# Kernel optimization log

Hardware: AMD Instinct MI355X
Metric: run time of the kernel (lower is better)

## Reference

```python
import jax, jax.numpy as jnp
import numpy as np

N, M, D = 4096, 8192, 512

def setup_inputs() -> dict:
    key = jax.random.key(0)
    k1, k2, k3, k4 = jax.random.split(key, 4)
    X = jax.random.normal(k1, (N, D), dtype=jnp.float32)
    SV = jax.random.normal(k2, (M, D), dtype=jnp.float32)
    DC = jax.random.normal(k3, (1, M), dtype=jnp.float32)
    IC = jax.random.normal(k4, (1,), dtype=jnp.float32)
    gamma = jnp.float32(1.0 / D)
    return {"X": X, "SV": SV, "DC": DC, "IC": IC, "gamma": gamma}

def reference(X, SV, DC, IC, gamma):
    # Squared pairwise L2 distances via GEMM expansion (same math as
    # ||SV - x||^2 without materializing the [N, M, D] broadcast tensor):
    # d2[n, m] = ||x_n||^2 + ||sv_m||^2 - 2 * x_n . sv_m
    x2 = jnp.sum(X * X, axis=1)          # [N]
    sv2 = jnp.sum(SV * SV, axis=1)       # [M]
    cross = jnp.einsum("nd,md->nm", X, SV)  # [N, M]
    d2 = jnp.maximum(x2[:, None] + sv2[None, :] - 2.0 * cross, 0.0)
    k = jnp.exp(-gamma * d2)             # RBF kernel values [N, M]
    # Weighted reduction over support vectors + intercept -> decision values [N]
    return jnp.sum(k * DC, axis=1) + IC
```

## Files before the change

### kernel.cpp

```cpp
#include <hip/hip_runtime.h>
#include <stdint.h>

#define NN 4096
#define MM 8192
#define DD 512
#define KT2 16

typedef __bf16 bf16x8 __attribute__((ext_vector_type(8)));
typedef __bf16 bf16x4 __attribute__((ext_vector_type(4)));
typedef float f32x4 __attribute__((ext_vector_type(4)));
typedef float f32x16 __attribute__((ext_vector_type(16)));

__device__ __forceinline__ void load_lds16(const void* g, void* l) {
  __builtin_amdgcn_global_load_lds(
      (const __attribute__((address_space(1))) unsigned int*)g,
      (__attribute__((address_space(3))) unsigned int*)l, 16, 0, 0);
}

__global__ __launch_bounds__(256) void convert_norm_kernel(
    const float* __restrict__ X, const float* __restrict__ SV,
    __bf16* __restrict__ Xb, __bf16* __restrict__ SVb,
    float* __restrict__ x2, float* __restrict__ sv2,
    float* __restrict__ out, const float* __restrict__ IC) {
  int wid = blockIdx.x * 4 + (threadIdx.x >> 6);
  int lane = threadIdx.x & 63;
  const float* src;
  __bf16* dst;
  float* nrm;
  if (wid < NN) {
    src = X + (size_t)wid * DD;
    dst = Xb + (size_t)wid * DD;
    nrm = x2 + wid;
    if (lane == 0) out[wid] = IC[0];
  } else {
    int r = wid - NN;
    src = SV + (size_t)r * DD;
    dst = SVb + (size_t)r * DD;
    nrm = sv2 + r;
  }
  const f32x4* s = (const f32x4*)src;
  f32x4 a = s[lane];
  f32x4 b = s[lane + 64];
  float sum = a.x * a.x + a.y * a.y + a.z * a.z + a.w * a.w +
              b.x * b.x + b.y * b.y + b.z * b.z + b.w * b.w;
  bf16x4 ca = {(__bf16)a.x, (__bf16)a.y, (__bf16)a.z, (__bf16)a.w};
  bf16x4 cb = {(__bf16)b.x, (__bf16)b.y, (__bf16)b.z, (__bf16)b.w};
  *(bf16x4*)(dst + 4 * lane) = ca;
  *(bf16x4*)(dst + 256 + 4 * lane) = cb;
#pragma unroll
  for (int m = 32; m >= 1; m >>= 1) sum += __shfl_xor(sum, m, 64);
  if (lane == 0) *nrm = sum;
}

__global__ __launch_bounds__(256, 4) void rbf_gemm_kernel(
    const bf16x8* __restrict__ Xb, const bf16x8* __restrict__ SVb,
    const float* __restrict__ x2, const float* __restrict__ sv2,
    const float* __restrict__ DC, const float* __restrict__ gamma_p,
    float* __restrict__ out) {
  __shared__ bf16x8 As[2][512];
  __shared__ bf16x8 Bs[2][512];

  const int t = threadIdx.x;
  const int lane = t & 63;
  const int wave = t >> 6;
  const int n0 = blockIdx.x * 128;
  const int m0 = blockIdx.y * 128;

  const int wave_m = wave & 1;
  const int wave_n = wave >> 1;
  const int l31 = lane & 31;
  const int lhi = lane >> 5;

  const int c0 = t;
  const int c1 = t + 256;
  const int r0 = c0 >> 2, k0 = (c0 & 3) ^ (r0 & 3);
  const int r1 = c1 >> 2, k1 = (c1 & 3) ^ (r1 & 3);
  const size_t gA0 = (size_t)(n0 + r0) * 64 + k0;
  const size_t gA1 = (size_t)(n0 + r1) * 64 + k1;
  const size_t gB0 = (size_t)(m0 + r0) * 64 + k0;
  const size_t gB1 = (size_t)(m0 + r1) * 64 + k1;

  const int ra4 = (wave_n * 64 + l31) * 4;
  const int rb4 = (wave_m * 64 + l31) * 4;

  f32x16 acc[2][2];
#pragma unroll
  for (int i = 0; i < 2; ++i)
#pragma unroll
    for (int j = 0; j < 2; ++j)
#pragma unroll
      for (int r = 0; r < 16; ++r) acc[i][j][r] = 0.0f;

  load_lds16(Xb + gA0, &As[0][c0]);
  load_lds16(Xb + gA1, &As[0][c1]);
  load_lds16(SVb + gB0, &Bs[0][c0]);
  load_lds16(SVb + gB1, &Bs[0][c1]);
  __syncthreads();

#pragma unroll
  for (int kt = 0; kt < KT2; ++kt) {
    const int cur = kt & 1;
    const int nxt = cur ^ 1;
    if (kt + 1 < KT2) {
      const int ko = (kt + 1) * 4;
      load_lds16(Xb + gA0 + ko, &As[nxt][c0]);
      load_lds16(Xb + gA1 + ko, &As[nxt][c1]);
      load_lds16(SVb + gB0 + ko, &Bs[nxt][c0]);
      load_lds16(SVb + gB1 + ko, &Bs[nxt][c1]);
    }
#pragma unroll
    for (int ks = 0; ks < 2; ++ks) {
      const int kc = ks * 2 + lhi;
      const int sw = kc ^ (l31 & 3);
      bf16x8 af0 = As[cur][ra4 + sw];
      bf16x8 af1 = As[cur][ra4 + 128 + sw];
      bf16x8 bf0 = Bs[cur][rb4 + sw];
      bf16x8 bf1 = Bs[cur][rb4 + 128 + sw];
      acc[0][0] = __builtin_amdgcn_mfma_f32_32x32x16_bf16(af0, bf0, acc[0][0], 0, 0, 0);
      acc[0][1] = __builtin_amdgcn_mfma_f32_32x32x16_bf16(af0, bf1, acc[0][1], 0, 0, 0);
      acc[1][0] = __builtin_amdgcn_mfma_f32_32x32x16_bf16(af1, bf0, acc[1][0], 0, 0, 0);
      acc[1][1] = __builtin_amdgcn_mfma_f32_32x32x16_bf16(af1, bf1, acc[1][1], 0, 0, 0);
    }
    __syncthreads();
  }

  const float g = gamma_p[0];
  const float c2 = g * 1.4426950408889634f;

  float sv2v[2], dcv[2];
  const int colb = m0 + wave_m * 64 + l31;
  sv2v[0] = sv2[colb];
  dcv[0] = DC[colb];
  sv2v[1] = sv2[colb + 32];
  dcv[1] = DC[colb + 32];

#pragma unroll
  for (int i = 0; i < 2; ++i) {
    const int rowb = n0 + wave_n * 64 + i * 32 + 4 * lhi;
    float val[16];
#pragma unroll
    for (int g4 = 0; g4 < 4; ++g4) {
      f32x4 xv = *(const f32x4*)(x2 + rowb + 8 * g4);
#pragma unroll
      for (int r2 = 0; r2 < 4; ++r2) {
        const int reg = g4 * 4 + r2;
        float v = 0.0f;
#pragma unroll
        for (int j = 0; j < 2; ++j) {
          float d2 = xv[r2] + sv2v[j] - 2.0f * acc[i][j][reg];
          d2 = fmaxf(d2, 0.0f);
          v += exp2f(-c2 * d2) * dcv[j];
        }
        val[reg] = v;
      }
    }
#pragma unroll
    for (int m = 1; m < 32; m <<= 1)
#pragma unroll
      for (int reg = 0; reg < 16; ++reg)
        val[reg] += __shfl_xor(val[reg], m, 64);
    if (l31 == 0) {
#pragma unroll
      for (int g4 = 0; g4 < 4; ++g4)
#pragma unroll
        for (int r2 = 0; r2 < 4; ++r2)
          atomicAdd(&out[rowb + 8 * g4 + r2], val[g4 * 4 + r2]);
    }
  }
}

extern "C" void kernel_launch(void* const* d_in, const int* in_sizes, int n_in,
                              void* d_out, int out_size, void* d_ws, size_t ws_size,
                              hipStream_t stream) {
  const float* X = (const float*)d_in[0];
  const float* SV = (const float*)d_in[1];
  const float* DC = (const float*)d_in[2];
  const float* IC = (const float*)d_in[3];
  const float* gamma = (const float*)d_in[4];
  float* out = (float*)d_out;

  char* ws = (char*)d_ws;
  __bf16* Xb = (__bf16*)ws;
  __bf16* SVb = (__bf16*)(ws + (size_t)NN * DD * 2);
  float* x2 = (float*)(ws + (size_t)(NN + MM) * DD * 2);
  float* sv2 = x2 + NN;

  convert_norm_kernel<<<(NN + MM) / 4, 256, 0, stream>>>(X, SV, Xb, SVb, x2, sv2, out, IC);
  dim3 grid(NN / 128, MM / 128);
  rbf_gemm_kernel<<<grid, 256, 0, stream>>>((const bf16x8*)Xb, (const bf16x8*)SVb,
                                            x2, sv2, DC, gamma, out);
}
```

Measured before the change: 144.5 us.

## Double block M-tile to 256 rows with 512 threads and pair-row LDS swizzle

Each workgroup of the fused bf16 MFMA GEMM now covers 256 rows of X instead of 128 and runs 8 waves instead of 4. Each SV tile loaded into LDS is therefore shared by twice as many rows, which cuts global B-tile traffic and halves the number of blocks. The LDS XOR swizzle now keys on row pairs, (row>>1)&3, rather than row&3, to change the bank-access pattern on fragment reads. In exchange, the 512-thread launch bound with 4 blocks per CU caps registers per thread, and the larger LDS footprint may lower occupancy.

Result: no change. 143.8 us (-0.5%).

```diff
diff --git a/kernel.cpp b/kernel.cpp
--- a/kernel.cpp
+++ b/kernel.cpp
@@ -4,7 +4,7 @@
 #define NN 4096
 #define MM 8192
 #define DD 512
-#define KT2 16
+#define KT3 16
 
 typedef __bf16 bf16x8 __attribute__((ext_vector_type(8)));
 typedef __bf16 bf16x4 __attribute__((ext_vector_type(4)));
@@ -52,18 +52,18 @@
   if (lane == 0) *nrm = sum;
 }
 
-__global__ __launch_bounds__(256, 4) void rbf_gemm_kernel(
+__global__ __launch_bounds__(512, 4) void rbf_gemm_kernel(
     const bf16x8* __restrict__ Xb, const bf16x8* __restrict__ SVb,
     const float* __restrict__ x2, const float* __restrict__ sv2,
     const float* __restrict__ DC, const float* __restrict__ gamma_p,
     float* __restrict__ out) {
-  __shared__ bf16x8 As[2][512];
+  __shared__ bf16x8 As[2][1024];
   __shared__ bf16x8 Bs[2][512];
 
   const int t = threadIdx.x;
   const int lane = t & 63;
   const int wave = t >> 6;
-  const int n0 = blockIdx.x * 128;
+  const int n0 = blockIdx.x * 256;
   const int m0 = blockIdx.y * 128;
 
   const int wave_m = wave & 1;
@@ -71,17 +71,17 @@
   const int l31 = lane & 31;
   const int lhi = lane >> 5;
 
-  const int c0 = t;
-  const int c1 = t + 256;
-  const int r0 = c0 >> 2, k0 = (c0 & 3) ^ (r0 & 3);
-  const int r1 = c1 >> 2, k1 = (c1 & 3) ^ (r1 & 3);
-  const size_t gA0 = (size_t)(n0 + r0) * 64 + k0;
-  const size_t gA1 = (size_t)(n0 + r1) * 64 + k1;
-  const size_t gB0 = (size_t)(m0 + r0) * 64 + k0;
-  const size_t gB1 = (size_t)(m0 + r1) * 64 + k1;
+  const int cA0 = t, cA1 = t + 512, cB0 = t;
+  const int rA0 = cA0 >> 2, kA0 = (cA0 & 3) ^ ((rA0 >> 1) & 3);
+  const int rA1 = cA1 >> 2, kA1 = (cA1 & 3) ^ ((rA1 >> 1) & 3);
+  const int rB0 = cB0 >> 2, kB0 = (cB0 & 3) ^ ((rB0 >> 1) & 3);
+  const size_t gA0 = (size_t)(n0 + rA0) * 64 + kA0;
+  const size_t gA1 = (size_t)(n0 + rA1) * 64 + kA1;
+  const size_t gB0 = (size_t)(m0 + rB0) * 64 + kB0;
 
   const int ra4 = (wave_n * 64 + l31) * 4;
   const int rb4 = (wave_m * 64 + l31) * 4;
+  const int swb = (l31 >> 1) & 3;
 
   f32x16 acc[2][2];
 #pragma unroll
@@ -91,27 +91,25 @@
 #pragma unroll
       for (int r = 0; r < 16; ++r) acc[i][j][r] = 0.0f;
 
-  load_lds16(Xb + gA0, &As[0][c0]);
-  load_lds16(Xb + gA1, &As[0][c1]);
-  load_lds16(SVb + gB0, &Bs[0][c0]);
-  load_lds16(SVb + gB1, &Bs[0][c1]);
+  load_lds16(Xb + gA0, &As[0][cA0]);
+  load_lds16(Xb + gA1, &As[0][cA1]);
+  load_lds16(SVb + gB0, &Bs[0][cB0]);
   __syncthreads();
 
 #pragma unroll
-  for (int kt = 0; kt < KT2; ++kt) {
+  for (int kt = 0; kt < KT3; ++kt) {
     const int cur = kt & 1;
     const int nxt = cur ^ 1;
-    if (kt + 1 < KT2) {
-      const int ko = (kt + 1) * 4;
-      load_lds16(Xb + gA0 + ko, &As[nxt][c0]);
-      load_lds16(Xb + gA1 + ko, &As[nxt][c1]);
-      load_lds16(SVb + gB0 + ko, &Bs[nxt][c0]);
-      load_lds16(SVb + gB1 + ko, &Bs[nxt][c1]);
+    if (kt + 1 < KT3) {
+      const size_t ko = (size_t)(kt + 1) * 4;
+      load_lds16(Xb + gA0 + ko, &As[nxt][cA0]);
+      load_lds16(Xb + gA1 + ko, &As[nxt][cA1]);
+      load_lds16(SVb + gB0 + ko, &Bs[nxt][cB0]);
     }
 #pragma unroll
     for (int ks = 0; ks < 2; ++ks) {
       const int kc = ks * 2 + lhi;
-      const int sw = kc ^ (l31 & 3);
+      const int sw = kc ^ swb;
       bf16x8 af0 = As[cur][ra4 + sw];
       bf16x8 af1 = As[cur][ra4 + 128 + sw];
       bf16x8 bf0 = Bs[cur][rb4 + sw];
@@ -186,7 +184,7 @@
   float* sv2 = x2 + NN;
 
   convert_norm_kernel<<<(NN + MM) / 4, 256, 0, stream>>>(X, SV, Xb, SVb, x2, sv2, out, IC);
-  dim3 grid(NN / 128, MM / 128);
-  rbf_gemm_kernel<<<grid, 256, 0, stream>>>((const bf16x8*)Xb, (const bf16x8*)SVb,
+  dim3 grid(NN / 256, MM / 128);
+  rbf_gemm_kernel<<<grid, 512, 0, stream>>>((const bf16x8*)Xb, (const bf16x8*)SVb,
                                             x2, sv2, DC, gamma, out);
 }
```
